# Kernel tuning notes

Hardware: AMD Instinct MI355X
Metric: run time of the kernel (lower is better)

The kernel has to match this reference:

```python
import jax, jax.numpy as jnp
import numpy as np


def setup_inputs() -> dict:
    key = jax.random.key(0)
    B, H, C, T = 8, 8, 64, 2048
    qkv = jax.random.normal(key, (B, 3 * H * C, T), dtype=jnp.float32)
    return {"qkv": qkv, "n_heads": H}


def reference(qkv, n_heads):
    # qkv: (B, 3*H*C, T)
    bs, width, length = qkv.shape
    ch = width // (3 * n_heads)
    q, k, v = jnp.split(qkv, 3, axis=1)          # each (B, H*C, T)
    scale = ch ** (-0.25)
    q = (q * scale).reshape(bs * n_heads, ch, length)
    k = (k * scale).reshape(bs * n_heads, ch, length)
    v = v.reshape(bs * n_heads, ch, length)
    # weight[b, t, s] = sum_c q[b,c,t] * k[b,c,s]
    weight = jnp.einsum('bct,bcs->bts', q, k)
    weight = jax.nn.softmax(weight.astype(jnp.float32), axis=-1).astype(qkv.dtype)
    out = jnp.einsum('bts,bcs->bct', weight, v)   # (B*H, C, T)
    return out.reshape(bs, n_heads * ch, length)
```

## Files before the change

kernel.cpp:

```cpp
#include <hip/hip_runtime.h>

typedef __bf16 bf16x4 __attribute__((ext_vector_type(4)));
typedef __bf16 bf16x8 __attribute__((ext_vector_type(8)));
typedef float floatx4 __attribute__((ext_vector_type(4)));
typedef float floatx16 __attribute__((ext_vector_type(16)));

#define T_SEQ 2048
#define TTILE 512
#define STILE 64
#define LOG2E_SCALE 0.18033688011112042f

__device__ __forceinline__ unsigned pack_bf16_pair(float a, float b) {
    unsigned ua = __builtin_bit_cast(unsigned, a) + 0x8000u;
    unsigned ub = __builtin_bit_cast(unsigned, b) + 0x8000u;
    return __builtin_amdgcn_perm(ub, ua, 0x07060302u);
}
__device__ __forceinline__ unsigned short bf16_bits(float a) {
    return (unsigned short)((__builtin_bit_cast(unsigned, a) + 0x8000u) >> 16);
}

__global__ __launch_bounds__(512, 2) void attn_fused(
    const float* __restrict__ qkv, float* __restrict__ out)
{
    __shared__ __align__(16) __bf16 Kt[STILE][72];
    __shared__ __align__(16) __bf16 Vs[64][72];

    const int tid  = threadIdx.x;
    const int lane = tid & 63;
    const int wave = tid >> 6;
    const int l31  = lane & 31;
    const int g    = lane >> 5;

    const int bh = blockIdx.y;
    const int b = bh >> 3, head = bh & 7;
    const size_t in_base = ((size_t)b * 1536 + head * 64) * T_SEQ;
    const float* Qg = qkv + in_base;
    const float* Kg = qkv + in_base + (size_t)512 * T_SEQ;
    const float* Vg = qkv + in_base + (size_t)1024 * T_SEQ;

    const int tcol0 = blockIdx.x * TTILE + wave * 64 + l31;
    const int tcol1 = tcol0 + 32;

    bf16x8 qf[2][4];
    #pragma unroll
    for (int kb = 0; kb < 4; ++kb)
        #pragma unroll
        for (int j = 0; j < 8; ++j) {
            size_t rowoff = (size_t)(kb * 16 + g * 8 + j) * T_SEQ;
            qf[0][kb][j] = (__bf16)(Qg[rowoff + tcol0] * LOG2E_SCALE);
            qf[1][kb][j] = (__bf16)(Qg[rowoff + tcol1] * LOG2E_SCALE);
        }

    union { unsigned u[4]; bf16x8 v; } ones;
    {
        unsigned pat = (l31 == 0) ? 0x3F803F80u : 0u;
        ones.u[0] = pat; ones.u[1] = pat; ones.u[2] = pat; ones.u[3] = pat;
    }

    floatx16 Oa[2][2];
    floatx16 La[2];
    #pragma unroll
    for (int tt = 0; tt < 2; ++tt) {
        #pragma unroll
        for (int r = 0; r < 16; ++r) { Oa[tt][0][r] = 0.0f; Oa[tt][1][r] = 0.0f; La[tt][r] = 0.0f; }
    }

    int cc[2], ss[2];
    size_t goff[2];
    #pragma unroll
    for (int r = 0; r < 2; ++r) {
        int i = tid + r * 512;
        cc[r] = i >> 4;
        ss[r] = (i & 15) * 4;
        goff[r] = (size_t)cc[r] * T_SEQ + ss[r];
    }
    const int ph = (tid >> 1) & 3;

    floatx4 kr[2], vr[2];
    #pragma unroll
    for (int r = 0; r < 2; ++r) {
        kr[r] = *(const floatx4*)(Kg + goff[r]);
        vr[r] = *(const floatx4*)(Vg + goff[r]);
    }

    for (int s0 = 0; s0 < T_SEQ; s0 += STILE) {
        __syncthreads();
        #pragma unroll
        for (int r = 0; r < 2; ++r) {
            int c = cc[r], s4 = ss[r];
            #pragma unroll
            for (int k = 0; k < 4; ++k) {
                int d = (k + ph) & 3;
                *(unsigned short*)&Kt[s4 + d][c] = bf16_bits(kr[r][d]);
            }
            unsigned v01 = pack_bf16_pair(vr[r][0], vr[r][1]);
            unsigned v23 = pack_bf16_pair(vr[r][2], vr[r][3]);
            union { unsigned u[2]; bf16x4 v; } vb;
            vb.u[0] = v01; vb.u[1] = v23;
            *(bf16x4*)&Vs[c][s4] = vb.v;
        }
        __syncthreads();

        if (s0 + STILE < T_SEQ) {
            #pragma unroll
            for (int r = 0; r < 2; ++r) {
                kr[r] = *(const floatx4*)(Kg + goff[r] + s0 + STILE);
                vr[r] = *(const floatx4*)(Vg + goff[r] + s0 + STILE);
            }
        }

        bf16x8 pf[2][4];
        #pragma unroll
        for (int ms = 0; ms < 2; ++ms) {
            floatx16 Sa0, Sa1;
            #pragma unroll
            for (int r = 0; r < 16; ++r) { Sa0[r] = 0.0f; Sa1[r] = 0.0f; }
            #pragma unroll
            for (int kb = 0; kb < 4; ++kb) {
                bf16x8 kf = *(const bf16x8*)&Kt[ms * 32 + l31][kb * 16 + g * 8];
                Sa0 = __builtin_amdgcn_mfma_f32_32x32x16_bf16(kf, qf[0][kb], Sa0, 0, 0, 0);
                Sa1 = __builtin_amdgcn_mfma_f32_32x32x16_bf16(kf, qf[1][kb], Sa1, 0, 0, 0);
            }
            #pragma unroll
            for (int tt = 0; tt < 2; ++tt) {
                const floatx16& Sa = tt ? Sa1 : Sa0;
                float p[16];
                #pragma unroll
                for (int r = 0; r < 16; ++r)
                    p[r] = __builtin_amdgcn_exp2f(Sa[r]);
                unsigned d[8];
                #pragma unroll
                for (int q = 0; q < 8; ++q) d[q] = pack_bf16_pair(p[2 * q], p[2 * q + 1]);
                #pragma unroll
                for (int kb = 0; kb < 2; ++kb) {
                    unsigned d0 = d[4 * kb + 0], d1 = d[4 * kb + 1];
                    unsigned d2 = d[4 * kb + 2], d3 = d[4 * kb + 3];
                    unsigned sendA = g ? d0 : d2;
                    unsigned sendB = g ? d1 : d3;
                    unsigned recvA = (unsigned)__shfl_xor((int)sendA, 32);
                    unsigned recvB = (unsigned)__shfl_xor((int)sendB, 32);
                    union { unsigned u[4]; bf16x8 v; } fu;
                    fu.u[0] = g ? recvA : d0;
                    fu.u[1] = g ? recvB : d1;
                    fu.u[2] = g ? d2    : recvA;
                    fu.u[3] = g ? d3    : recvB;
                    pf[tt][ms * 2 + kb] = fu.v;
                }
            }
        }

        #pragma unroll
        for (int mc = 0; mc < 2; ++mc)
            #pragma unroll
            for (int kb2 = 0; kb2 < 4; ++kb2) {
                bf16x8 vf = *(const bf16x8*)&Vs[mc * 32 + l31][kb2 * 16 + g * 8];
                Oa[0][mc] = __builtin_amdgcn_mfma_f32_32x32x16_bf16(vf, pf[0][kb2], Oa[0][mc], 0, 0, 0);
                Oa[1][mc] = __builtin_amdgcn_mfma_f32_32x32x16_bf16(vf, pf[1][kb2], Oa[1][mc], 0, 0, 0);
            }
        #pragma unroll
        for (int kb2 = 0; kb2 < 4; ++kb2) {
            La[0] = __builtin_amdgcn_mfma_f32_32x32x16_bf16(ones.v, pf[0][kb2], La[0], 0, 0, 0);
            La[1] = __builtin_amdgcn_mfma_f32_32x32x16_bf16(ones.v, pf[1][kb2], La[1], 0, 0, 0);
        }
    }

    float d0 = La[0][0], d1 = La[1][0];
    float rl0 = 1.0f / (d0 + __shfl_xor(d0, 32));
    float rl1 = 1.0f / (d1 + __shfl_xor(d1, 32));

    const size_t out_base = ((size_t)b * 512 + head * 64) * T_SEQ;
    #pragma unroll
    for (int mc = 0; mc < 2; ++mc)
        #pragma unroll
        for (int r = 0; r < 16; ++r) {
            int c = mc * 32 + (r & 3) + 8 * (r >> 2) + 4 * g;
            size_t row = out_base + (size_t)c * T_SEQ;
            out[row + tcol0] = Oa[0][mc][r] * rl0;
            out[row + tcol1] = Oa[1][mc][r] * rl1;
        }
}

extern "C" void kernel_launch(void* const* d_in, const int* in_sizes, int n_in,
                              void* d_out, int out_size, void* d_ws, size_t ws_size,
                              hipStream_t stream) {
    const float* qkv = (const float*)d_in[0];
    float* out = (float*)d_out;
    dim3 grid(T_SEQ / TTILE, 64);
    attn_fused<<<grid, dim3(512), 0, stream>>>(qkv, out);
}
```

Baseline: 210.3 us.

## Double-buffer K/V shared tiles and merge row-sum MFMAs into one accumulator

K and V tiles now live in two shared-memory buffers, so each iteration needs a single barrier and the LDS stores for the next tile happen after the current tile's compute. The row-sum accumulation for both query sub-tiles goes into one accumulator, using two ones-vectors that place the two sums in different rows, which frees 16 accumulator registers. The first QK MFMA also uses a shared zero vector in place of re-zeroing each time. The cost is doubled LDS use, which still fits two blocks per CU, and a longer dependency chain on the single La accumulator.

```diff
diff --git a/kernel.cpp b/kernel.cpp
--- a/kernel.cpp
+++ b/kernel.cpp
@@ -22,8 +22,8 @@
 __global__ __launch_bounds__(512, 2) void attn_fused(
     const float* __restrict__ qkv, float* __restrict__ out)
 {
-    __shared__ __align__(16) __bf16 Kt[STILE][72];
-    __shared__ __align__(16) __bf16 Vs[64][72];
+    __shared__ __align__(16) __bf16 Kt[2][STILE][72];
+    __shared__ __align__(16) __bf16 Vs[2][64][72];
 
     const int tid  = threadIdx.x;
     const int lane = tid & 63;
@@ -51,19 +51,22 @@
             qf[1][kb][j] = (__bf16)(Qg[rowoff + tcol1] * LOG2E_SCALE);
         }
 
-    union { unsigned u[4]; bf16x8 v; } ones;
+    floatx16 zf;
+    #pragma unroll
+    for (int r = 0; r < 16; ++r) zf[r] = 0.0f;
+
+    union U4 { unsigned u[4]; bf16x8 v; };
+    U4 one0, one1;
     {
-        unsigned pat = (l31 == 0) ? 0x3F803F80u : 0u;
-        ones.u[0] = pat; ones.u[1] = pat; ones.u[2] = pat; ones.u[3] = pat;
+        unsigned p0 = (l31 == 0) ? 0x3F803F80u : 0u;
+        unsigned p1 = (l31 == 1) ? 0x3F803F80u : 0u;
+        one0.u[0] = p0; one0.u[1] = p0; one0.u[2] = p0; one0.u[3] = p0;
+        one1.u[0] = p1; one1.u[1] = p1; one1.u[2] = p1; one1.u[3] = p1;
     }
 
     floatx16 Oa[2][2];
-    floatx16 La[2];
-    #pragma unroll
-    for (int tt = 0; tt < 2; ++tt) {
-        #pragma unroll
-        for (int r = 0; r < 16; ++r) { Oa[tt][0][r] = 0.0f; Oa[tt][1][r] = 0.0f; La[tt][r] = 0.0f; }
-    }
+    floatx16 La = zf;
+    Oa[0][0] = zf; Oa[0][1] = zf; Oa[1][0] = zf; Oa[1][1] = zf;
 
     int cc[2], ss[2];
     size_t goff[2];
@@ -82,42 +85,50 @@
         kr[r] = *(const floatx4*)(Kg + goff[r]);
         vr[r] = *(const floatx4*)(Vg + goff[r]);
     }
-
-    for (int s0 = 0; s0 < T_SEQ; s0 += STILE) {
+    #pragma unroll
+    for (int r = 0; r < 2; ++r) {
+        int c = cc[r], s4 = ss[r];
+        #pragma unroll
+        for (int k = 0; k < 4; ++k) {
+            int d = (k + ph) & 3;
+            *(unsigned short*)&Kt[0][s4 + d][c] = bf16_bits(kr[r][d]);
+        }
+        union { unsigned u[2]; bf16x4 v; } vb;
+        vb.u[0] = pack_bf16_pair(vr[r][0], vr[r][1]);
+        vb.u[1] = pack_bf16_pair(vr[r][2], vr[r][3]);
+        *(bf16x4*)&Vs[0][c][s4] = vb.v;
+    }
+
+    for (int it = 0; it < T_SEQ / STILE; ++it) {
+        const int rb = it & 1;
+        const int s_next = (it + 1) * STILE;
+        const bool pref = (s_next < T_SEQ);
+
         __syncthreads();
-        #pragma unroll
-        for (int r = 0; r < 2; ++r) {
-            int c = cc[r], s4 = ss[r];
-            #pragma unroll
-            for (int k = 0; k < 4; ++k) {
-                int d = (k + ph) & 3;
-                *(unsigned short*)&Kt[s4 + d][c] = bf16_bits(kr[r][d]);
-            }
-            unsigned v01 = pack_bf16_pair(vr[r][0], vr[r][1]);
-            unsigned v23 = pack_bf16_pair(vr[r][2], vr[r][3]);
-            union { unsigned u[2]; bf16x4 v; } vb;
-            vb.u[0] = v01; vb.u[1] = v23;
-            *(bf16x4*)&Vs[c][s4] = vb.v;
-        }
-        __syncthreads();
-
-        if (s0 + STILE < T_SEQ) {
+
+        if (pref) {
             #pragma unroll
             for (int r = 0; r < 2; ++r) {
-                kr[r] = *(const floatx4*)(Kg + goff[r] + s0 + STILE);
-                vr[r] = *(const floatx4*)(Vg + goff[r] + s0 + STILE);
-            }
-        }
+                kr[r] = *(const floatx4*)(Kg + goff[r] + s_next);
+                vr[r] = *(const floatx4*)(Vg + goff[r] + s_next);
+            }
+        }
+
+        const __bf16 (*KtR)[72] = Kt[rb];
+        const __bf16 (*VsR)[72] = Vs[rb];
 
         bf16x8 pf[2][4];
         #pragma unroll
         for (int ms = 0; ms < 2; ++ms) {
             floatx16 Sa0, Sa1;
-            #pragma unroll
-            for (int r = 0; r < 16; ++r) { Sa0[r] = 0.0f; Sa1[r] = 0.0f; }
-            #pragma unroll
-            for (int kb = 0; kb < 4; ++kb) {
-                bf16x8 kf = *(const bf16x8*)&Kt[ms * 32 + l31][kb * 16 + g * 8];
+            {
+                bf16x8 kf = *(const bf16x8*)&KtR[ms * 32 + l31][g * 8];
+                Sa0 = __builtin_amdgcn_mfma_f32_32x32x16_bf16(kf, qf[0][0], zf, 0, 0, 0);
+                Sa1 = __builtin_amdgcn_mfma_f32_32x32x16_bf16(kf, qf[1][0], zf, 0, 0, 0);
+            }
+            #pragma unroll
+            for (int kb = 1; kb < 4; ++kb) {
+                bf16x8 kf = *(const bf16x8*)&KtR[ms * 32 + l31][kb * 16 + g * 8];
                 Sa0 = __builtin_amdgcn_mfma_f32_32x32x16_bf16(kf, qf[0][kb], Sa0, 0, 0, 0);
                 Sa1 = __builtin_amdgcn_mfma_f32_32x32x16_bf16(kf, qf[1][kb], Sa1, 0, 0, 0);
             }
@@ -153,18 +164,36 @@
         for (int mc = 0; mc < 2; ++mc)
             #pragma unroll
             for (int kb2 = 0; kb2 < 4; ++kb2) {
-                bf16x8 vf = *(const bf16x8*)&Vs[mc * 32 + l31][kb2 * 16 + g * 8];
+                bf16x8 vf = *(const bf16x8*)&VsR[mc * 32 + l31][kb2 * 16 + g * 8];
                 Oa[0][mc] = __builtin_amdgcn_mfma_f32_32x32x16_bf16(vf, pf[0][kb2], Oa[0][mc], 0, 0, 0);
                 Oa[1][mc] = __builtin_amdgcn_mfma_f32_32x32x16_bf16(vf, pf[1][kb2], Oa[1][mc], 0, 0, 0);
             }
         #pragma unroll
         for (int kb2 = 0; kb2 < 4; ++kb2) {
-            La[0] = __builtin_amdgcn_mfma_f32_32x32x16_bf16(ones.v, pf[0][kb2], La[0], 0, 0, 0);
-            La[1] = __builtin_amdgcn_mfma_f32_32x32x16_bf16(ones.v, pf[1][kb2], La[1], 0, 0, 0);
-        }
-    }
-
-    float d0 = La[0][0], d1 = La[1][0];
+            La = __builtin_amdgcn_mfma_f32_32x32x16_bf16(one0.v, pf[0][kb2], La, 0, 0, 0);
+            La = __builtin_amdgcn_mfma_f32_32x32x16_bf16(one1.v, pf[1][kb2], La, 0, 0, 0);
+        }
+
+        if (pref) {
+            __bf16 (*KtW)[72] = Kt[rb ^ 1];
+            __bf16 (*VsW)[72] = Vs[rb ^ 1];
+            #pragma unroll
+            for (int r = 0; r < 2; ++r) {
+                int c = cc[r], s4 = ss[r];
+                #pragma unroll
+                for (int k = 0; k < 4; ++k) {
+                    int d = (k + ph) & 3;
+                    *(unsigned short*)&KtW[s4 + d][c] = bf16_bits(kr[r][d]);
+                }
+                union { unsigned u[2]; bf16x4 v; } vb;
+                vb.u[0] = pack_bf16_pair(vr[r][0], vr[r][1]);
+                vb.u[1] = pack_bf16_pair(vr[r][2], vr[r][3]);
+                *(bf16x4*)&VsW[c][s4] = vb.v;
+            }
+        }
+    }
+
+    float d0 = La[0], d1 = La[1];
     float rl0 = 1.0f / (d0 + __shfl_xor(d0, 32));
     float rl1 = 1.0f / (d1 + __shfl_xor(d1, 32));
 
```

Result: no change. 209.0 us (-0.6%).
